# Kernel tuning notes

Measured on AMD Instinct MI355X. Metric: run time of the kernel, lower is better.

## Reference

```python
import jax, jax.numpy as jnp
import numpy as np

L = 2          # layer_num
B = 8192       # nframes * nloc
NNEI = 128
EMB = 128
HID = 128
SHIFT = 20.0   # attnw_shift default
SCALING = (HID * 1.0) ** (-0.5)
LN_EPS = 1e-5


def _l2norm(x):
    # torch F.normalize: x / max(||x||, 1e-12)
    n = jnp.sqrt(jnp.sum(x * x, axis=-1, keepdims=True))
    return x / jnp.maximum(n, 1e-12)


def _layernorm(x, g, b):
    mu = jnp.mean(x, axis=-1, keepdims=True)
    var = jnp.mean((x - mu) ** 2, axis=-1, keepdims=True)
    return (x - mu) * jax.lax.rsqrt(var + LN_EPS) * g + b


def setup_inputs() -> dict:
    key = jax.random.key(0)
    ks = jax.random.split(key, 10)
    input_G = jax.random.normal(ks[0], (B, NNEI, EMB), dtype=jnp.float32)
    nei_mask = jax.random.randint(ks[1], (B, NNEI), 0, 2) > 0
    input_r = jax.random.normal(ks[2], (B, NNEI, 3), dtype=jnp.float32)
    input_r = _l2norm(input_r)  # normalized radial vectors
    sw = jax.random.uniform(ks[3], (B, NNEI), dtype=jnp.float32)
    s = 0.02
    W_in = jax.random.normal(ks[4], (L, EMB, 3 * HID), dtype=jnp.float32) * s
    b_in = jnp.zeros((L, 3 * HID), dtype=jnp.float32)
    W_out = jax.random.normal(ks[5], (L, HID, EMB), dtype=jnp.float32) * s
    b_out = jnp.zeros((L, EMB), dtype=jnp.float32)
    ln_g = jnp.ones((L, EMB), dtype=jnp.float32)
    ln_b = jnp.zeros((L, EMB), dtype=jnp.float32)
    return {"input_G": input_G, "nei_mask": nei_mask, "input_r": input_r,
            "sw": sw, "W_in": W_in, "b_in": b_in, "W_out": W_out,
            "b_out": b_out, "ln_g": ln_g, "ln_b": ln_b}


def reference(input_G, nei_mask, input_r, sw, W_in, b_in, W_out, b_out, ln_g, ln_b):
    # smooth=True, dotr=True path of NeighborGatedAttention
    sw_ij = sw[:, :, None] * sw[:, None, :]                     # [B, nnei, nnei]
    ang = jnp.einsum('bnc,bmc->bnm', input_r, input_r)          # angular weight
    x = input_G
    for l in range(L):
        residual = x
        qkv = jnp.einsum('bne,eh->bnh', x, W_in[l]) + b_in[l]
        q, k, v = jnp.split(qkv, 3, axis=-1)
        q = _l2norm(q) * SCALING
        k = _l2norm(k)
        v = _l2norm(v)
        attn = jnp.einsum('bnh,bmh->bnm', q, k)
        attn = (attn + SHIFT) * sw_ij - SHIFT                   # switch smoothing
        attn = jax.nn.softmax(attn, axis=-1)
        attn = jnp.where(nei_mask[:, :, None], attn, 0.0)       # zero masked rows
        attn = attn * sw_ij * ang                               # smooth + dotr
        o = jnp.einsum('bnm,bmh->bnh', attn, v)
        out = jnp.einsum('bnh,he->bne', o, W_out[l]) + b_out[l]
        x = _layernorm(residual + out, ln_g[l], ln_b[l])
    return x
```

## Files before the change

kernel.cpp:

```cpp
#include <hip/hip_runtime.h>
#include <hip/hip_bf16.h>
#include <math.h>


typedef __attribute__((ext_vector_type(8))) short bf16x8;
typedef __attribute__((ext_vector_type(4))) float f32x4;
typedef unsigned short ushort_t;

constexpr float F_SHIFT   = 20.0f;
constexpr float F_SCALING = 0.08838834764831845f;
constexpr float F_LNEPS   = 1e-5f;

constexpr int ROWP = 136;
constexpr int BUF_US = 128 * ROWP;
constexpr size_t WTI_ELEMS = 2 * 384 * 128;
constexpr size_t WTO_ELEMS = 2 * 128 * 128;
constexpr int TAB_F = 1920;
constexpr int LDS_BYTES = 4 * BUF_US * 2 + 2 * TAB_F * 4;

#define MFMA(a, b, c) __builtin_amdgcn_mfma_f32_16x16x32_bf16(a, b, c, 0, 0, 0)

__device__ __forceinline__ ushort_t f2bf(float f) {
  __hip_bfloat16 h = __float2bfloat16(f);
  return *reinterpret_cast<ushort_t*>(&h);
}
__device__ __forceinline__ ushort4 pack4(float a, float b, float c, float d) {
  return make_ushort4(f2bf(a), f2bf(b), f2bf(c), f2bf(d));
}

template <bool WS>
__device__ __forceinline__ bf16x8 wt_frag(const ushort_t* __restrict__ wt,
                                          const float* __restrict__ W,
                                          int r, int c, int ldW) {
  if constexpr (WS) {
    return *(const bf16x8*)(wt + r * 128 + c);
  } else {
    bf16x8 f;
#pragma unroll
    for (int j = 0; j < 8; ++j) f[j] = (short)f2bf(W[(size_t)(c + j) * ldW + r]);
    return f;
  }
}

__global__ void prep_weights(const float* __restrict__ Win, const float* __restrict__ Wout,
                             ushort_t* __restrict__ wtI, ushort_t* __restrict__ wtO) {
  const int i = blockIdx.x * 256 + threadIdx.x;
  if (i < (int)WTI_ELEMS) {
    const int l = i / (384 * 128), r = i % (384 * 128), h = r >> 7, e = r & 127;
    wtI[i] = f2bf(Win[l * (128 * 384) + e * 384 + h]);
  }
  if (i < (int)WTO_ELEMS) {
    const int l = i >> 14, r = i & 16383, e = r >> 7, h = r & 127;
    wtO[i] = f2bf(Wout[(l << 14) + h * 128 + e]);
  }
}

__device__ __forceinline__ bf16x8 load_xf(const float* xr) {
  const float4 a = *(const float4*)xr;
  const float4 c = *(const float4*)(xr + 4);
  bf16x8 f;
  f[0] = (short)f2bf(a.x); f[1] = (short)f2bf(a.y);
  f[2] = (short)f2bf(a.z); f[3] = (short)f2bf(a.w);
  f[4] = (short)f2bf(c.x); f[5] = (short)f2bf(c.y);
  f[6] = (short)f2bf(c.z); f[7] = (short)f2bf(c.w);
  return f;
}

template <bool WS>
__global__ __launch_bounds__(512, 2)
void ngatt_dual(const float* __restrict__ G, const int* __restrict__ nmask,
                const float* __restrict__ r3, const float* __restrict__ swg,
                const float* __restrict__ Win, const float* __restrict__ bin,
                const float* __restrict__ Wout, const float* __restrict__ bout,
                const float* __restrict__ lng, const float* __restrict__ lnb,
                const ushort_t* __restrict__ wtin, const ushort_t* __restrict__ wtout,
                float* __restrict__ xout) {
  extern __shared__ char smem[];
  ushort_t* bufA0 = (ushort_t*)smem;
  ushort_t* bufB0 = bufA0 + BUF_US;
  ushort_t* bufA1 = bufB0 + BUF_US;
  ushort_t* bufB1 = bufA1 + BUF_US;
  float* tab0 = (float*)(bufB1 + BUF_US);
  float* tab1 = tab0 + TAB_F;

  const int bid = blockIdx.x, t = threadIdx.x;
  const int w = t >> 6, l = t & 63, lc = l & 15, lg = l >> 4;
  const int b0 = 2 * bid, b1 = b0 + 1;
  const size_t bb0 = (size_t)b0 * (128 * 128);
  const size_t bb1 = (size_t)b1 * (128 * 128);
  const int n_mine = 16 * w + lc;

  if (t < 256) {
    const int tb = t >> 7, tt = t & 127;
    float* T = tb ? tab1 : tab0;
    const size_t gi = (size_t)(b0 + tb) * 128 + tt;
    T[1280 + tt] = swg[gi];
    T[1408 + tt] = nmask[gi] ? 1.0f : 0.0f;
    T[1536 + tt] = r3[gi * 3 + 0];
    T[1664 + tt] = r3[gi * 3 + 1];
    T[1792 + tt] = r3[gi * 3 + 2];
  }
  __syncthreads();

  for (int layer = 0; layer < 2; ++layer) {
    const float* xsrc0 = layer ? (xout + bb0) : (G + bb0);
    const float* xsrc1 = layer ? (xout + bb1) : (G + bb1);
    const ushort_t* wtI = wtin + (size_t)layer * 384 * 128;
    const ushort_t* wtO = wtout + (size_t)layer * 128 * 128;
    const float* WinL  = Win  + (size_t)layer * 128 * 384;
    const float* WoutL = Wout + (size_t)layer * 128 * 128;
    const float* binL  = bin  + layer * 384;
    const float* boutL = bout + layer * 128;
    const float* lngL  = lng  + layer * 128;
    const float* lnbL  = lnb  + layer * 128;

    bf16x8 xf0[4], xf1[4];
#pragma unroll
    for (int kk = 0; kk < 4; ++kk) {
      xf0[kk] = load_xf(xsrc0 + (size_t)n_mine * 128 + 8 * lg + 32 * kk);
      xf1[kk] = load_xf(xsrc1 + (size_t)n_mine * 128 + 8 * lg + 32 * kk);
    }

    float ssq0 = 0.f, ssq1 = 0.f, ssk0 = 0.f, ssk1 = 0.f;
#pragma unroll 2
    for (int i = 0; i < 8; ++i) {
      bf16x8 aw[4];
#pragma unroll
      for (int kk = 0; kk < 4; ++kk)
        aw[kk] = wt_frag<WS>(wtI, WinL, 16 * i + lc, 8 * lg + 32 * kk, 384);
      f32x4 a0 = {0, 0, 0, 0}, a1 = {0, 0, 0, 0};
#pragma unroll
      for (int kk = 0; kk < 4; ++kk) {
        a0 = MFMA(aw[kk], xf0[kk], a0);
        a1 = MFMA(aw[kk], xf1[kk], a1);
      }
      const float4 bi = *(const float4*)&binL[16 * i + 4 * lg];
      {
        const float v0 = a0[0] + bi.x, v1 = a0[1] + bi.y, v2 = a0[2] + bi.z, v3 = a0[3] + bi.w;
        ssq0 += v0 * v0 + v1 * v1 + v2 * v2 + v3 * v3;
        *(ushort4*)(bufA0 + n_mine * ROWP + 16 * i + 4 * lg) = pack4(v0, v1, v2, v3);
      }
      {
        const float v0 = a1[0] + bi.x, v1 = a1[1] + bi.y, v2 = a1[2] + bi.z, v3 = a1[3] + bi.w;
        ssq1 += v0 * v0 + v1 * v1 + v2 * v2 + v3 * v3;
        *(ushort4*)(bufA1 + n_mine * ROWP + 16 * i + 4 * lg) = pack4(v0, v1, v2, v3);
      }
    }
#pragma unroll 2
    for (int i = 0; i < 8; ++i) {
      bf16x8 aw[4];
#pragma unroll
      for (int kk = 0; kk < 4; ++kk)
        aw[kk] = wt_frag<WS>(wtI, WinL, 128 + 16 * i + lc, 8 * lg + 32 * kk, 384);
      f32x4 a0 = {0, 0, 0, 0}, a1 = {0, 0, 0, 0};
#pragma unroll
      for (int kk = 0; kk < 4; ++kk) {
        a0 = MFMA(aw[kk], xf0[kk], a0);
        a1 = MFMA(aw[kk], xf1[kk], a1);
      }
      const float4 bi = *(const float4*)&binL[128 + 16 * i + 4 * lg];
      {
        const float v0 = a0[0] + bi.x, v1 = a0[1] + bi.y, v2 = a0[2] + bi.z, v3 = a0[3] + bi.w;
        ssk0 += v0 * v0 + v1 * v1 + v2 * v2 + v3 * v3;
        *(ushort4*)(bufB0 + n_mine * ROWP + 16 * i + 4 * lg) = pack4(v0, v1, v2, v3);
      }
      {
        const float v0 = a1[0] + bi.x, v1 = a1[1] + bi.y, v2 = a1[2] + bi.z, v3 = a1[3] + bi.w;
        ssk1 += v0 * v0 + v1 * v1 + v2 * v2 + v3 * v3;
        *(ushort4*)(bufB1 + n_mine * ROWP + 16 * i + 4 * lg) = pack4(v0, v1, v2, v3);
      }
    }
    ssq0 += __shfl_xor(ssq0, 16); ssq0 += __shfl_xor(ssq0, 32);
    ssq1 += __shfl_xor(ssq1, 16); ssq1 += __shfl_xor(ssq1, 32);
    ssk0 += __shfl_xor(ssk0, 16); ssk0 += __shfl_xor(ssk0, 32);
    ssk1 += __shfl_xor(ssk1, 16); ssk1 += __shfl_xor(ssk1, 32);
    if (l < 16) {
      tab0[0 + n_mine] = ssq0; tab0[128 + n_mine] = ssk0;
      tab1[0 + n_mine] = ssq1; tab1[128 + n_mine] = ssk1;
    }
    __syncthreads();

    if (t < 256) {
      const int tb = t >> 7, tt = t & 127;
      float* T = tb ? tab1 : tab0;
      T[0 + tt] = 1.0f / fmaxf(sqrtf(T[0 + tt]), 1e-12f);
      T[512 + 4 * tt + 0] = (1.0f / fmaxf(sqrtf(T[128 + tt]), 1e-12f)) * F_SCALING;
      T[512 + 4 * tt + 1] = T[1280 + tt];
      T[512 + 4 * tt + 2] = 0.0f;
      T[512 + 4 * tt + 3] = T[1536 + tt];
      T[1024 + 2 * tt + 0] = T[1664 + tt];
      T[1024 + 2 * tt + 1] = T[1792 + tt];
    }
    bf16x8 qf0[4], qf1[4];
#pragma unroll
    for (int kk = 0; kk < 4; ++kk) {
      qf0[kk] = *(const bf16x8*)(bufA0 + n_mine * ROWP + 8 * lg + 32 * kk);
      qf1[kk] = *(const bf16x8*)(bufA1 + n_mine * ROWP + 8 * lg + 32 * kk);
    }
    __syncthreads();

    float ssv0 = 0.f, ssv1 = 0.f;
#pragma unroll 2
    for (int i = 0; i < 8; ++i) {
      bf16x8 aw[4];
#pragma unroll
      for (int kk = 0; kk < 4; ++kk)
        aw[kk] = wt_frag<WS>(wtI, WinL, 256 + 16 * i + lc, 8 * lg + 32 * kk, 384);
      f32x4 a0 = {0, 0, 0, 0}, a1 = {0, 0, 0, 0};
#pragma unroll
      for (int kk = 0; kk < 4; ++kk) {
        a0 = MFMA(aw[kk], xf0[kk], a0);
        a1 = MFMA(aw[kk], xf1[kk], a1);
      }
      const float4 bi = *(const float4*)&binL[256 + 16 * i + 4 * lg];
      {
        const float v0 = a0[0] + bi.x, v1 = a0[1] + bi.y, v2 = a0[2] + bi.z, v3 = a0[3] + bi.w;
        ssv0 += v0 * v0 + v1 * v1 + v2 * v2 + v3 * v3;
        *(ushort4*)(bufA0 + n_mine * ROWP + 16 * i + 4 * lg) = pack4(v0, v1, v2, v3);
      }
      {
        const float v0 = a1[0] + bi.x, v1 = a1[1] + bi.y, v2 = a1[2] + bi.z, v3 = a1[3] + bi.w;
        ssv1 += v0 * v0 + v1 * v1 + v2 * v2 + v3 * v3;
        *(ushort4*)(bufA1 + n_mine * ROWP + 16 * i + 4 * lg) = pack4(v0, v1, v2, v3);
      }
    }
    ssv0 += __shfl_xor(ssv0, 16); ssv0 += __shfl_xor(ssv0, 32);
    ssv1 += __shfl_xor(ssv1, 16); ssv1 += __shfl_xor(ssv1, 32);
    if (l < 16) { tab0[256 + n_mine] = ssv0; tab1[256 + n_mine] = ssv1; }

    f32x4 sacc0[8], sacc1[8];
    float fac0, fac1;
    {
      const float iqn = tab0[0 + n_mine];
      const float swn = tab0[1280 + n_mine];
      const float rxn = tab0[1536 + n_mine], ryn = tab0[1664 + n_mine], rzn = tab0[1792 + n_mine];
      float sum = 0.0f;
#pragma unroll 2
      for (int mt = 0; mt < 8; ++mt) {
        bf16x8 kf[4];
#pragma unroll
        for (int kk = 0; kk < 4; ++kk)
          kf[kk] = *(const bf16x8*)(bufB0 + (16 * mt + lc) * ROWP + 8 * lg + 32 * kk);
        f32x4 a = {0, 0, 0, 0};
#pragma unroll
        for (int kk = 0; kk < 4; ++kk) a = MFMA(kf[kk], qf0[kk], a);
#pragma unroll
        for (int r2 = 0; r2 < 4; ++r2) {
          const int m = 16 * mt + 4 * lg + r2;
          const float4 a4 = *(const float4*)&tab0[512 + 4 * m];
          const float2 b2 = *(const float2*)&tab0[1024 + 2 * m];
          const float sws = swn * a4.y;
          const float e = __expf((a[r2] * iqn * a4.x + F_SHIFT) * sws - F_SHIFT);
          sum += e;
          a[r2] = e * sws * (rxn * a4.w + ryn * b2.x + rzn * b2.y);
        }
        sacc0[mt] = a;
      }
      sum += __shfl_xor(sum, 16); sum += __shfl_xor(sum, 32);
      fac0 = tab0[1408 + n_mine] / sum;
    }
    {
      const float iqn = tab1[0 + n_mine];
      const float swn = tab1[1280 + n_mine];
      const float rxn = tab1[1536 + n_mine], ryn = tab1[1664 + n_mine], rzn = tab1[1792 + n_mine];
      float sum = 0.0f;
#pragma unroll 2
      for (int mt = 0; mt < 8; ++mt) {
        bf16x8 kf[4];
#pragma unroll
        for (int kk = 0; kk < 4; ++kk)
          kf[kk] = *(const bf16x8*)(bufB1 + (16 * mt + lc) * ROWP + 8 * lg + 32 * kk);
        f32x4 a = {0, 0, 0, 0};
#pragma unroll
        for (int kk = 0; kk < 4; ++kk) a = MFMA(kf[kk], qf1[kk], a);
#pragma unroll
        for (int r2 = 0; r2 < 4; ++r2) {
          const int m = 16 * mt + 4 * lg + r2;
          const float4 a4 = *(const float4*)&tab1[512 + 4 * m];
          const float2 b2 = *(const float2*)&tab1[1024 + 2 * m];
          const float sws = swn * a4.y;
          const float e = __expf((a[r2] * iqn * a4.x + F_SHIFT) * sws - F_SHIFT);
          sum += e;
          a[r2] = e * sws * (rxn * a4.w + ryn * b2.x + rzn * b2.y);
        }
        sacc1[mt] = a;
      }
      sum += __shfl_xor(sum, 16); sum += __shfl_xor(sum, 32);
      fac1 = tab1[1408 + n_mine] / sum;
    }
    __syncthreads();

    if (t < 256) {
      const int tb = t >> 7, tt = t & 127;
      float* T = tb ? tab1 : tab0;
      T[384 + tt] = 1.0f / fmaxf(sqrtf(T[256 + tt]), 1e-12f);
    }
#pragma unroll
    for (int mt = 0; mt < 8; ++mt) {
      *(ushort4*)(bufB0 + n_mine * ROWP + 16 * mt + 4 * lg) =
          pack4(sacc0[mt][0] * fac0, sacc0[mt][1] * fac0, sacc0[mt][2] * fac0, sacc0[mt][3] * fac0);
      *(ushort4*)(bufB1 + n_mine * ROWP + 16 * mt + 4 * lg) =
          pack4(sacc1[mt][0] * fac1, sacc1[mt][1] * fac1, sacc1[mt][2] * fac1, sacc1[mt][3] * fac1);
    }
    bf16x8 vf0[4], vf1[4];
#pragma unroll
    for (int kk = 0; kk < 4; ++kk) {
      vf0[kk] = *(const bf16x8*)(bufA0 + n_mine * ROWP + 8 * lg + 32 * kk);
      vf1[kk] = *(const bf16x8*)(bufA1 + n_mine * ROWP + 8 * lg + 32 * kk);
    }
    __syncthreads();

    bf16x8 pf0[4], pf1[4];
#pragma unroll
    for (int kk = 0; kk < 4; ++kk) {
      pf0[kk] = *(const bf16x8*)(bufB0 + n_mine * ROWP + 8 * lg + 32 * kk);
      pf1[kk] = *(const bf16x8*)(bufB1 + n_mine * ROWP + 8 * lg + 32 * kk);
    }

    {
      const float4 iv0 = *(const float4*)&tab0[384 + 16 * w + 4 * lg];
      const float4 iv1 = *(const float4*)&tab1[384 + 16 * w + 4 * lg];
#pragma unroll 2
      for (int i = 0; i < 8; ++i) {
        bf16x8 bw[4];
#pragma unroll
        for (int kk = 0; kk < 4; ++kk)
          bw[kk] = wt_frag<WS>(wtO, WoutL, 16 * i + lc, 8 * lg + 32 * kk, 128);
        f32x4 a0 = {0, 0, 0, 0}, a1 = {0, 0, 0, 0};
#pragma unroll
        for (int kk = 0; kk < 4; ++kk) {
          a0 = MFMA(vf0[kk], bw[kk], a0);
          a1 = MFMA(vf1[kk], bw[kk], a1);
        }
        *(ushort4*)(bufA0 + (16 * i + lc) * ROWP + 16 * w + 4 * lg) =
            pack4(a0[0] * iv0.x, a0[1] * iv0.y, a0[2] * iv0.z, a0[3] * iv0.w);
        *(ushort4*)(bufA1 + (16 * i + lc) * ROWP + 16 * w + 4 * lg) =
            pack4(a1[0] * iv1.x, a1[1] * iv1.y, a1[2] * iv1.z, a1[3] * iv1.w);
      }
    }
    __syncthreads();

    float bo8[8], g8[8], be8[8];
#pragma unroll
    for (int ct = 0; ct < 8; ++ct) {
      const int e = 16 * ct + lc;
      bo8[ct] = boutL[e]; g8[ct] = lngL[e]; be8[ct] = lnbL[e];
    }
#pragma unroll 1
    for (int which = 0; which < 2; ++which) {
      const ushort_t* bufA = which ? bufA1 : bufA0;
      const float* xsrc = which ? xsrc1 : xsrc0;
      float* xo = xout + (which ? bb1 : bb0);
      f32x4 oacc[8];
#pragma unroll 2
      for (int i = 0; i < 8; ++i) {
        bf16x8 bf[4];
#pragma unroll
        for (int kk = 0; kk < 4; ++kk)
          bf[kk] = *(const bf16x8*)(bufA + (16 * i + lc) * ROWP + 8 * lg + 32 * kk);
        f32x4 a = {0, 0, 0, 0};
        if (which == 0) {
#pragma unroll
          for (int kk = 0; kk < 4; ++kk) a = MFMA(pf0[kk], bf[kk], a);
        } else {
#pragma unroll
          for (int kk = 0; kk < 4; ++kk) a = MFMA(pf1[kk], bf[kk], a);
        }
        oacc[i] = a;
      }
#pragma unroll
      for (int r2 = 0; r2 < 4; ++r2) {
        const int n = 16 * w + 4 * lg + r2;
        const float* xr = xsrc + (size_t)n * 128;
        float vals[8];
        float s1 = 0.0f, s2 = 0.0f;
#pragma unroll
        for (int ct = 0; ct < 8; ++ct) {
          const float v = oacc[ct][r2] + bo8[ct] + xr[16 * ct + lc];
          vals[ct] = v; s1 += v; s2 += v * v;
        }
        s1 += __shfl_xor(s1, 1); s1 += __shfl_xor(s1, 2);
        s1 += __shfl_xor(s1, 4); s1 += __shfl_xor(s1, 8);
        s2 += __shfl_xor(s2, 1); s2 += __shfl_xor(s2, 2);
        s2 += __shfl_xor(s2, 4); s2 += __shfl_xor(s2, 8);
        const float mu = s1 * (1.0f / 128.0f);
        const float rs = rsqrtf(s2 * (1.0f / 128.0f) - mu * mu + F_LNEPS);
        float* orow = xo + (size_t)n * 128;
#pragma unroll
        for (int ct = 0; ct < 8; ++ct)
          orow[16 * ct + lc] = (vals[ct] - mu) * rs * g8[ct] + be8[ct];
      }
    }
    __syncthreads();
  }
}

extern "C" void kernel_launch(void* const* d_in, const int* in_sizes, int n_in,
                              void* d_out, int out_size, void* d_ws, size_t ws_size,
                              hipStream_t stream) {
  const float* G    = (const float*)d_in[0];
  const int*   msk  = (const int*)d_in[1];
  const float* r3   = (const float*)d_in[2];
  const float* swg  = (const float*)d_in[3];
  const float* Win  = (const float*)d_in[4];
  const float* bin  = (const float*)d_in[5];
  const float* Wout = (const float*)d_in[6];
  const float* bout = (const float*)d_in[7];
  const float* lng  = (const float*)d_in[8];
  const float* lnb  = (const float*)d_in[9];
  float* xout = (float*)d_out;

  const int B = in_sizes[0] / (128 * 128);
  const int nblk = B / 2;
  const bool ws_ok = ws_size >= (WTI_ELEMS + WTO_ELEMS) * sizeof(ushort_t);
  ushort_t* wtI = (ushort_t*)d_ws;
  ushort_t* wtO = wtI + WTI_ELEMS;

  if (ws_ok) {
    prep_weights<<<dim3(384), dim3(256), 0, stream>>>(Win, Wout, wtI, wtO);
    hipFuncSetAttribute(reinterpret_cast<const void*>(ngatt_dual<true>),
                        hipFuncAttributeMaxDynamicSharedMemorySize, LDS_BYTES);
    ngatt_dual<true><<<dim3(nblk), dim3(512), LDS_BYTES, stream>>>(
        G, msk, r3, swg, Win, bin, Wout, bout, lng, lnb, wtI, wtO, xout);
  } else {
    hipFuncSetAttribute(reinterpret_cast<const void*>(ngatt_dual<false>),
                        hipFuncAttributeMaxDynamicSharedMemorySize, LDS_BYTES);
    ngatt_dual<false><<<dim3(nblk), dim3(512), LDS_BYTES, stream>>>(
        G, msk, r3, swg, Win, bin, Wout, bout, lng, lnb, nullptr, nullptr, xout);
  }
}
```

Before: 1.735 ms.

## Software-pipeline weight fragment loads and interleave the two batch elements' MFMA chains

The QKV and output-projection loops now prefetch the next weight fragment into a second register set while the current fragments feed the MFMAs, so global or LDS weight latency overlaps with compute. The score/softmax loop and the final P·V projection loop now process both batch elements in one pass, giving two independent MFMA chains for more instruction-level parallelism. These changes raise register pressure (extra fragment buffers and a second set of oacc accumulators), which could lower occupancy or cause spills.

```diff
diff --git a/kernel.cpp b/kernel.cpp
--- a/kernel.cpp
+++ b/kernel.cpp
@@ -122,52 +122,70 @@
     }
 
     float ssq0 = 0.f, ssq1 = 0.f, ssk0 = 0.f, ssk1 = 0.f;
-#pragma unroll 2
-    for (int i = 0; i < 8; ++i) {
-      bf16x8 aw[4];
+    {
+      bf16x8 aw[4], nw[4];
 #pragma unroll
       for (int kk = 0; kk < 4; ++kk)
-        aw[kk] = wt_frag<WS>(wtI, WinL, 16 * i + lc, 8 * lg + 32 * kk, 384);
-      f32x4 a0 = {0, 0, 0, 0}, a1 = {0, 0, 0, 0};
-#pragma unroll
-      for (int kk = 0; kk < 4; ++kk) {
-        a0 = MFMA(aw[kk], xf0[kk], a0);
-        a1 = MFMA(aw[kk], xf1[kk], a1);
-      }
-      const float4 bi = *(const float4*)&binL[16 * i + 4 * lg];
-      {
-        const float v0 = a0[0] + bi.x, v1 = a0[1] + bi.y, v2 = a0[2] + bi.z, v3 = a0[3] + bi.w;
-        ssq0 += v0 * v0 + v1 * v1 + v2 * v2 + v3 * v3;
-        *(ushort4*)(bufA0 + n_mine * ROWP + 16 * i + 4 * lg) = pack4(v0, v1, v2, v3);
-      }
-      {
-        const float v0 = a1[0] + bi.x, v1 = a1[1] + bi.y, v2 = a1[2] + bi.z, v3 = a1[3] + bi.w;
-        ssq1 += v0 * v0 + v1 * v1 + v2 * v2 + v3 * v3;
-        *(ushort4*)(bufA1 + n_mine * ROWP + 16 * i + 4 * lg) = pack4(v0, v1, v2, v3);
-      }
-    }
-#pragma unroll 2
-    for (int i = 0; i < 8; ++i) {
-      bf16x8 aw[4];
+        aw[kk] = wt_frag<WS>(wtI, WinL, lc, 8 * lg + 32 * kk, 384);
+#pragma unroll 1
+      for (int i = 0; i < 8; ++i) {
+        if (i < 7) {
+#pragma unroll
+          for (int kk = 0; kk < 4; ++kk)
+            nw[kk] = wt_frag<WS>(wtI, WinL, 16 * (i + 1) + lc, 8 * lg + 32 * kk, 384);
+        }
+        f32x4 a0 = {0, 0, 0, 0}, a1 = {0, 0, 0, 0};
+#pragma unroll
+        for (int kk = 0; kk < 4; ++kk) {
+          a0 = MFMA(aw[kk], xf0[kk], a0);
+          a1 = MFMA(aw[kk], xf1[kk], a1);
+        }
+        const float4 bi = *(const float4*)&binL[16 * i + 4 * lg];
+        {
+          const float v0 = a0[0] + bi.x, v1 = a0[1] + bi.y, v2 = a0[2] + bi.z, v3 = a0[3] + bi.w;
+          ssq0 += v0 * v0 + v1 * v1 + v2 * v2 + v3 * v3;
+          *(ushort4*)(bufA0 + n_mine * ROWP + 16 * i + 4 * lg) = pack4(v0, v1, v2, v3);
+        }
+        {
+          const float v0 = a1[0] + bi.x, v1 = a1[1] + bi.y, v2 = a1[2] + bi.z, v3 = a1[3] + bi.w;
+          ssq1 += v0 * v0 + v1 * v1 + v2 * v2 + v3 * v3;
+          *(ushort4*)(bufA1 + n_mine * ROWP + 16 * i + 4 * lg) = pack4(v0, v1, v2, v3);
+        }
+#pragma unroll
+        for (int kk = 0; kk < 4; ++kk) aw[kk] = nw[kk];
+      }
+    }
+    {
+      bf16x8 aw[4], nw[4];
 #pragma unroll
       for (int kk = 0; kk < 4; ++kk)
-        aw[kk] = wt_frag<WS>(wtI, WinL, 128 + 16 * i + lc, 8 * lg + 32 * kk, 384);
-      f32x4 a0 = {0, 0, 0, 0}, a1 = {0, 0, 0, 0};
-#pragma unroll
-      for (int kk = 0; kk < 4; ++kk) {
-        a0 = MFMA(aw[kk], xf0[kk], a0);
-        a1 = MFMA(aw[kk], xf1[kk], a1);
-      }
-      const float4 bi = *(const float4*)&binL[128 + 16 * i + 4 * lg];
-      {
-        const float v0 = a0[0] + bi.x, v1 = a0[1] + bi.y, v2 = a0[2] + bi.z, v3 = a0[3] + bi.w;
-        ssk0 += v0 * v0 + v1 * v1 + v2 * v2 + v3 * v3;
-        *(ushort4*)(bufB0 + n_mine * ROWP + 16 * i + 4 * lg) = pack4(v0, v1, v2, v3);
-      }
-      {
-        const float v0 = a1[0] + bi.x, v1 = a1[1] + bi.y, v2 = a1[2] + bi.z, v3 = a1[3] + bi.w;
-        ssk1 += v0 * v0 + v1 * v1 + v2 * v2 + v3 * v3;
-        *(ushort4*)(bufB1 + n_mine * ROWP + 16 * i + 4 * lg) = pack4(v0, v1, v2, v3);
+        aw[kk] = wt_frag<WS>(wtI, WinL, 128 + lc, 8 * lg + 32 * kk, 384);
+#pragma unroll 1
+      for (int i = 0; i < 8; ++i) {
+        if (i < 7) {
+#pragma unroll
+          for (int kk = 0; kk < 4; ++kk)
+            nw[kk] = wt_frag<WS>(wtI, WinL, 128 + 16 * (i + 1) + lc, 8 * lg + 32 * kk, 384);
+        }
+        f32x4 a0 = {0, 0, 0, 0}, a1 = {0, 0, 0, 0};
+#pragma unroll
+        for (int kk = 0; kk < 4; ++kk) {
+          a0 = MFMA(aw[kk], xf0[kk], a0);
+          a1 = MFMA(aw[kk], xf1[kk], a1);
+        }
+        const float4 bi = *(const float4*)&binL[128 + 16 * i + 4 * lg];
+        {
+          const float v0 = a0[0] + bi.x, v1 = a0[1] + bi.y, v2 = a0[2] + bi.z, v3 = a0[3] + bi.w;
+          ssk0 += v0 * v0 + v1 * v1 + v2 * v2 + v3 * v3;
+          *(ushort4*)(bufB0 + n_mine * ROWP + 16 * i + 4 * lg) = pack4(v0, v1, v2, v3);
+        }
+        {
+          const float v0 = a1[0] + bi.x, v1 = a1[1] + bi.y, v2 = a1[2] + bi.z, v3 = a1[3] + bi.w;
+          ssk1 += v0 * v0 + v1 * v1 + v2 * v2 + v3 * v3;
+          *(ushort4*)(bufB1 + n_mine * ROWP + 16 * i + 4 * lg) = pack4(v0, v1, v2, v3);
+        }
+#pragma unroll
+        for (int kk = 0; kk < 4; ++kk) aw[kk] = nw[kk];
       }
     }
     ssq0 += __shfl_xor(ssq0, 16); ssq0 += __shfl_xor(ssq0, 32);
@@ -200,28 +218,37 @@
     __syncthreads();
 
     float ssv0 = 0.f, ssv1 = 0.f;
-#pragma unroll 2
-    for (int i = 0; i < 8; ++i) {
-      bf16x8 aw[4];
+    {
+      bf16x8 aw[4], nw[4];
 #pragma unroll
       for (int kk = 0; kk < 4; ++kk)
-        aw[kk] = wt_frag<WS>(wtI, WinL, 256 + 16 * i + lc, 8 * lg + 32 * kk, 384);
-      f32x4 a0 = {0, 0, 0, 0}, a1 = {0, 0, 0, 0};
-#pragma unroll
-      for (int kk = 0; kk < 4; ++kk) {
-        a0 = MFMA(aw[kk], xf0[kk], a0);
-        a1 = MFMA(aw[kk], xf1[kk], a1);
-      }
-      const float4 bi = *(const float4*)&binL[256 + 16 * i + 4 * lg];
-      {
-        const float v0 = a0[0] + bi.x, v1 = a0[1] + bi.y, v2 = a0[2] + bi.z, v3 = a0[3] + bi.w;
-        ssv0 += v0 * v0 + v1 * v1 + v2 * v2 + v3 * v3;
-        *(ushort4*)(bufA0 + n_mine * ROWP + 16 * i + 4 * lg) = pack4(v0, v1, v2, v3);
-      }
-      {
-        const float v0 = a1[0] + bi.x, v1 = a1[1] + bi.y, v2 = a1[2] + bi.z, v3 = a1[3] + bi.w;
-        ssv1 += v0 * v0 + v1 * v1 + v2 * v2 + v3 * v3;
-        *(ushort4*)(bufA1 + n_mine * ROWP + 16 * i + 4 * lg) = pack4(v0, v1, v2, v3);
+        aw[kk] = wt_frag<WS>(wtI, WinL, 256 + lc, 8 * lg + 32 * kk, 384);
+#pragma unroll 1
+      for (int i = 0; i < 8; ++i) {
+        if (i < 7) {
+#pragma unroll
+          for (int kk = 0; kk < 4; ++kk)
+            nw[kk] = wt_frag<WS>(wtI, WinL, 256 + 16 * (i + 1) + lc, 8 * lg + 32 * kk, 384);
+        }
+        f32x4 a0 = {0, 0, 0, 0}, a1 = {0, 0, 0, 0};
+#pragma unroll
+        for (int kk = 0; kk < 4; ++kk) {
+          a0 = MFMA(aw[kk], xf0[kk], a0);
+          a1 = MFMA(aw[kk], xf1[kk], a1);
+        }
+        const float4 bi = *(const float4*)&binL[256 + 16 * i + 4 * lg];
+        {
+          const float v0 = a0[0] + bi.x, v1 = a0[1] + bi.y, v2 = a0[2] + bi.z, v3 = a0[3] + bi.w;
+          ssv0 += v0 * v0 + v1 * v1 + v2 * v2 + v3 * v3;
+          *(ushort4*)(bufA0 + n_mine * ROWP + 16 * i + 4 * lg) = pack4(v0, v1, v2, v3);
+        }
+        {
+          const float v0 = a1[0] + bi.x, v1 = a1[1] + bi.y, v2 = a1[2] + bi.z, v3 = a1[3] + bi.w;
+          ssv1 += v0 * v0 + v1 * v1 + v2 * v2 + v3 * v3;
+          *(ushort4*)(bufA1 + n_mine * ROWP + 16 * i + 4 * lg) = pack4(v0, v1, v2, v3);
+        }
+#pragma unroll
+        for (int kk = 0; kk < 4; ++kk) aw[kk] = nw[kk];
       }
     }
     ssv0 += __shfl_xor(ssv0, 16); ssv0 += __shfl_xor(ssv0, 32);
@@ -231,62 +258,51 @@
     f32x4 sacc0[8], sacc1[8];
     float fac0, fac1;
     {
-      const float iqn = tab0[0 + n_mine];
-      const float swn = tab0[1280 + n_mine];
-      const float rxn = tab0[1536 + n_mine], ryn = tab0[1664 + n_mine], rzn = tab0[1792 + n_mine];
-      float sum = 0.0f;
+      const float iqn0 = tab0[0 + n_mine], iqn1 = tab1[0 + n_mine];
+      const float swn0 = tab0[1280 + n_mine], swn1 = tab1[1280 + n_mine];
+      const float rxn0 = tab0[1536 + n_mine], ryn0 = tab0[1664 + n_mine], rzn0 = tab0[1792 + n_mine];
+      const float rxn1 = tab1[1536 + n_mine], ryn1 = tab1[1664 + n_mine], rzn1 = tab1[1792 + n_mine];
+      float sum0 = 0.0f, sum1 = 0.0f;
 #pragma unroll 2
       for (int mt = 0; mt < 8; ++mt) {
-        bf16x8 kf[4];
-#pragma unroll
-        for (int kk = 0; kk < 4; ++kk)
-          kf[kk] = *(const bf16x8*)(bufB0 + (16 * mt + lc) * ROWP + 8 * lg + 32 * kk);
-        f32x4 a = {0, 0, 0, 0};
-#pragma unroll
-        for (int kk = 0; kk < 4; ++kk) a = MFMA(kf[kk], qf0[kk], a);
+        bf16x8 kf0[4], kf1[4];
+#pragma unroll
+        for (int kk = 0; kk < 4; ++kk) {
+          kf0[kk] = *(const bf16x8*)(bufB0 + (16 * mt + lc) * ROWP + 8 * lg + 32 * kk);
+          kf1[kk] = *(const bf16x8*)(bufB1 + (16 * mt + lc) * ROWP + 8 * lg + 32 * kk);
+        }
+        f32x4 a0 = {0, 0, 0, 0}, a1 = {0, 0, 0, 0};
+#pragma unroll
+        for (int kk = 0; kk < 4; ++kk) {
+          a0 = MFMA(kf0[kk], qf0[kk], a0);
+          a1 = MFMA(kf1[kk], qf1[kk], a1);
+        }
 #pragma unroll
         for (int r2 = 0; r2 < 4; ++r2) {
           const int m = 16 * mt + 4 * lg + r2;
-          const float4 a4 = *(const float4*)&tab0[512 + 4 * m];
-          const float2 b2 = *(const float2*)&tab0[1024 + 2 * m];
-          const float sws = swn * a4.y;
-          const float e = __expf((a[r2] * iqn * a4.x + F_SHIFT) * sws - F_SHIFT);
-          sum += e;
-          a[r2] = e * sws * (rxn * a4.w + ryn * b2.x + rzn * b2.y);
-        }
-        sacc0[mt] = a;
-      }
-      sum += __shfl_xor(sum, 16); sum += __shfl_xor(sum, 32);
-      fac0 = tab0[1408 + n_mine] / sum;
-    }
-    {
-      const float iqn = tab1[0 + n_mine];
-      const float swn = tab1[1280 + n_mine];
-      const float rxn = tab1[1536 + n_mine], ryn = tab1[1664 + n_mine], rzn = tab1[1792 + n_mine];
-      float sum = 0.0f;
-#pragma unroll 2
-      for (int mt = 0; mt < 8; ++mt) {
-        bf16x8 kf[4];
-#pragma unroll
-        for (int kk = 0; kk < 4; ++kk)
-          kf[kk] = *(const bf16x8*)(bufB1 + (16 * mt + lc) * ROWP + 8 * lg + 32 * kk);
-        f32x4 a = {0, 0, 0, 0};
-#pragma unroll
-        for (int kk = 0; kk < 4; ++kk) a = MFMA(kf[kk], qf1[kk], a);
-#pragma unroll
-        for (int r2 = 0; r2 < 4; ++r2) {
-          const int m = 16 * mt + 4 * lg + r2;
-          const float4 a4 = *(const float4*)&tab1[512 + 4 * m];
-          const float2 b2 = *(const float2*)&tab1[1024 + 2 * m];
-          const float sws = swn * a4.y;
-          const float e = __expf((a[r2] * iqn * a4.x + F_SHIFT) * sws - F_SHIFT);
-          sum += e;
-          a[r2] = e * sws * (rxn * a4.w + ryn * b2.x + rzn * b2.y);
-        }
-        sacc1[mt] = a;
-      }
-      sum += __shfl_xor(sum, 16); sum += __shfl_xor(sum, 32);
-      fac1 = tab1[1408 + n_mine] / sum;
+          {
+            const float4 a4 = *(const float4*)&tab0[512 + 4 * m];
+            const float2 b2 = *(const float2*)&tab0[1024 + 2 * m];
+            const float sws = swn0 * a4.y;
+            const float e = __expf((a0[r2] * iqn0 * a4.x + F_SHIFT) * sws - F_SHIFT);
+            sum0 += e;
+            a0[r2] = e * sws * (rxn0 * a4.w + ryn0 * b2.x + rzn0 * b2.y);
+          }
+          {
+            const float4 a4 = *(const float4*)&tab1[512 + 4 * m];
+            const float2 b2 = *(const float2*)&tab1[1024 + 2 * m];
+            const float sws = swn1 * a4.y;
+            const float e = __expf((a1[r2] * iqn1 * a4.x + F_SHIFT) * sws - F_SHIFT);
+            sum1 += e;
+            a1[r2] = e * sws * (rxn1 * a4.w + ryn1 * b2.x + rzn1 * b2.y);
+          }
+        }
+        sacc0[mt] = a0; sacc1[mt] = a1;
+      }
+      sum0 += __shfl_xor(sum0, 16); sum0 += __shfl_xor(sum0, 32);
+      sum1 += __shfl_xor(sum1, 16); sum1 += __shfl_xor(sum1, 32);
+      fac0 = tab0[1408 + n_mine] / sum0;
+      fac1 = tab1[1408 + n_mine] / sum1;
     }
     __syncthreads();
 
@@ -320,12 +336,17 @@
     {
       const float4 iv0 = *(const float4*)&tab0[384 + 16 * w + 4 * lg];
       const float4 iv1 = *(const float4*)&tab1[384 + 16 * w + 4 * lg];
-#pragma unroll 2
+      bf16x8 bw[4], nw[4];
+#pragma unroll
+      for (int kk = 0; kk < 4; ++kk)
+        bw[kk] = wt_frag<WS>(wtO, WoutL, lc, 8 * lg + 32 * kk, 128);
+#pragma unroll 1
       for (int i = 0; i < 8; ++i) {
-        bf16x8 bw[4];
-#pragma unroll
-        for (int kk = 0; kk < 4; ++kk)
-          bw[kk] = wt_frag<WS>(wtO, WoutL, 16 * i + lc, 8 * lg + 32 * kk, 128);
+        if (i < 7) {
+#pragma unroll
+          for (int kk = 0; kk < 4; ++kk)
+            nw[kk] = wt_frag<WS>(wtO, WoutL, 16 * (i + 1) + lc, 8 * lg + 32 * kk, 128);
+        }
         f32x4 a0 = {0, 0, 0, 0}, a1 = {0, 0, 0, 0};
 #pragma unroll
         for (int kk = 0; kk < 4; ++kk) {
@@ -336,59 +357,64 @@
             pack4(a0[0] * iv0.x, a0[1] * iv0.y, a0[2] * iv0.z, a0[3] * iv0.w);
         *(ushort4*)(bufA1 + (16 * i + lc) * ROWP + 16 * w + 4 * lg) =
             pack4(a1[0] * iv1.x, a1[1] * iv1.y, a1[2] * iv1.z, a1[3] * iv1.w);
-      }
-    }
-    __syncthreads();
-
-    float bo8[8], g8[8], be8[8];
-#pragma unroll
-    for (int ct = 0; ct < 8; ++ct) {
-      const int e = 16 * ct + lc;
-      bo8[ct] = boutL[e]; g8[ct] = lngL[e]; be8[ct] = lnbL[e];
-    }
+#pragma unroll
+        for (int kk = 0; kk < 4; ++kk) bw[kk] = nw[kk];
+      }
+    }
+    __syncthreads();
+
+    f32x4 oacc0[8], oacc1[8];
+#pragma unroll 2
+    for (int i = 0; i < 8; ++i) {
+      bf16x8 bf0[4], bf1[4];
+#pragma unroll
+      for (int kk = 0; kk < 4; ++kk) {
+        bf0[kk] = *(const bf16x8*)(bufA0 + (16 * i + lc) * ROWP + 8 * lg + 32 * kk);
+        bf1[kk] = *(const bf16x8*)(bufA1 + (16 * i + lc) * ROWP + 8 * lg + 32 * kk);
+      }
+      f32x4 a0 = {0, 0, 0, 0}, a1 = {0, 0, 0, 0};
+#pragma unroll
+      for (int kk = 0; kk < 4; ++kk) {
+        a0 = MFMA(pf0[kk], bf0[kk], a0);
+        a1 = MFMA(pf1[kk], bf1[kk], a1);
+      }
+      oacc0[i] = a0; oacc1[i] = a1;
+    }
+
+    {
+      float bo8[8], g8[8], be8[8];
+#pragma unroll
+      for (int ct = 0; ct < 8; ++ct) {
+        const int e = 16 * ct + lc;
+        bo8[ct] = boutL[e]; g8[ct] = lngL[e]; be8[ct] = lnbL[e];
+      }
 #pragma unroll 1
-    for (int which = 0; which < 2; ++which) {
-      const ushort_t* bufA = which ? bufA1 : bufA0;
-      const float* xsrc = which ? xsrc1 : xsrc0;
-      float* xo = xout + (which ? bb1 : bb0);
-      f32x4 oacc[8];
-#pragma unroll 2
-      for (int i = 0; i < 8; ++i) {
-        bf16x8 bf[4];
-#pragma unroll
-        for (int kk = 0; kk < 4; ++kk)
-          bf[kk] = *(const bf16x8*)(bufA + (16 * i + lc) * ROWP + 8 * lg + 32 * kk);
-        f32x4 a = {0, 0, 0, 0};
-        if (which == 0) {
-#pragma unroll
-          for (int kk = 0; kk < 4; ++kk) a = MFMA(pf0[kk], bf[kk], a);
-        } else {
-#pragma unroll
-          for (int kk = 0; kk < 4; ++kk) a = MFMA(pf1[kk], bf[kk], a);
-        }
-        oacc[i] = a;
-      }
-#pragma unroll
-      for (int r2 = 0; r2 < 4; ++r2) {
-        const int n = 16 * w + 4 * lg + r2;
-        const float* xr = xsrc + (size_t)n * 128;
-        float vals[8];
-        float s1 = 0.0f, s2 = 0.0f;
-#pragma unroll
-        for (int ct = 0; ct < 8; ++ct) {
-          const float v = oacc[ct][r2] + bo8[ct] + xr[16 * ct + lc];
-          vals[ct] = v; s1 += v; s2 += v * v;
-        }
-        s1 += __shfl_xor(s1, 1); s1 += __shfl_xor(s1, 2);
-        s1 += __shfl_xor(s1, 4); s1 += __shfl_xor(s1, 8);
-        s2 += __shfl_xor(s2, 1); s2 += __shfl_xor(s2, 2);
-        s2 += __shfl_xor(s2, 4); s2 += __shfl_xor(s2, 8);
-        const float mu = s1 * (1.0f / 128.0f);
-        const float rs = rsqrtf(s2 * (1.0f / 128.0f) - mu * mu + F_LNEPS);
-        float* orow = xo + (size_t)n * 128;
-#pragma unroll
-        for (int ct = 0; ct < 8; ++ct)
-          orow[16 * ct + lc] = (vals[ct] - mu) * rs * g8[ct] + be8[ct];
+      for (int which = 0; which < 2; ++which) {
+        const f32x4* oacc = which ? oacc1 : oacc0;
+        const float* xsrc = which ? xsrc1 : xsrc0;
+        float* xo = xout + (which ? bb1 : bb0);
+#pragma unroll
+        for (int r2 = 0; r2 < 4; ++r2) {
+          const int n = 16 * w + 4 * lg + r2;
+          const float* xr = xsrc + (size_t)n * 128;
+          float vals[8];
+          float s1 = 0.0f, s2 = 0.0f;
+#pragma unroll
+          for (int ct = 0; ct < 8; ++ct) {
+            const float v = oacc[ct][r2] + bo8[ct] + xr[16 * ct + lc];
+            vals[ct] = v; s1 += v; s2 += v * v;
+          }
+          s1 += __shfl_xor(s1, 1); s1 += __shfl_xor(s1, 2);
+          s1 += __shfl_xor(s1, 4); s1 += __shfl_xor(s1, 8);
+          s2 += __shfl_xor(s2, 1); s2 += __shfl_xor(s2, 2);
+          s2 += __shfl_xor(s2, 4); s2 += __shfl_xor(s2, 8);
+          const float mu = s1 * (1.0f / 128.0f);
+          const float rs = rsqrtf(s2 * (1.0f / 128.0f) - mu * mu + F_LNEPS);
+          float* orow = xo + (size_t)n * 128;
+#pragma unroll
+          for (int ct = 0; ct < 8; ++ct)
+            orow[16 * ct + lc] = (vals[ct] - mu) * rs * g8[ct] + be8[ct];
+        }
       }
     }
     __syncthreads();
```

New measurement: 2.591 ms. 1.49x slower.
